# Kernel optimization log

Measured on AMD Instinct MI355X. Metric: run time of the kernel, lower is better.

The kernel has to match this reference:

```python
import jax, jax.numpy as jnp
import numpy as np


def _shift_kernels():
    # [4,1,3,3] OIHW: left, right, up, down shift-difference kernels (as in torch module)
    kl = [[0, 0, 0], [-1, 1, 0], [0, 0, 0]]
    kr = [[0, 0, 0], [0, 1, -1], [0, 0, 0]]
    ku = [[0, -1, 0], [0, 1, 0], [0, 0, 0]]
    kd = [[0, 0, 0], [0, 1, 0], [0, -1, 0]]
    return jnp.asarray(np.stack([kl, kr, ku, kd])[:, None], dtype=jnp.float32)


def _avgpool4(x):
    # x: [B,1,H,W] -> [B,1,H//4,W//4], non-overlapping 4x4 mean (nn.AvgPool2d(4))
    b, c, h, w = x.shape
    return x.reshape(b, c, h // 4, 4, w // 4, 4).mean(axis=(3, 5))


def setup_inputs() -> dict:
    key = jax.random.key(0)
    k1, k2 = jax.random.split(key)
    org = jax.random.uniform(k1, (32, 3, 512, 512), dtype=jnp.float32)
    enhance = jax.random.uniform(k2, (32, 3, 512, 512), dtype=jnp.float32)
    return {"org": org, "enhance": enhance}


def reference(org, enhance):
    org_pool = _avgpool4(jnp.mean(org, axis=1, keepdims=True))
    enh_pool = _avgpool4(jnp.mean(enhance, axis=1, keepdims=True))
    # conv is linear, so D_org_k - D_enh_k == conv(org_pool - enh_pool, k).
    diff = org_pool - enh_pool  # [B,1,h,w]
    d = jax.lax.conv_general_dilated(
        diff, _shift_kernels(), window_strides=(1, 1),
        padding=((1, 1), (1, 1)),
        dimension_numbers=("NCHW", "OIHW", "NCHW"))  # [B,4,h,w]
    # torch: mean(D_left + D_right + D_up + D_down) over [B,1,h,w]
    return jnp.mean(jnp.sum(d * d, axis=1))
```

## Files before the change

kernel.cpp:

```cpp
#include <hip/hip_runtime.h>

#define NB 32
#define NC 3
#define NH 512
#define NW 512
#define PH 128
#define PW 128
#define NPOOL (NB * PH * PW)
#define NBLK_POOL (NPOOL / 256)
#define NBLK_RED  (NPOOL / 256)

__global__ __launch_bounds__(256) void pool_diff_kernel(
    const float* __restrict__ org, const float* __restrict__ enh,
    float* __restrict__ pooled)
{
    int idx = blockIdx.x * blockDim.x + threadIdx.x;
    int pw = idx & (PW - 1);
    int ph = (idx >> 7) & (PH - 1);
    int b  = idx >> 14;

    const float4* o4 = (const float4*)org;
    const float4* e4 = (const float4*)enh;
    const int rowF4 = NW / 4;
    const int chanF4 = NH * rowF4;

    int base = (b * NC * NH + 4 * ph) * rowF4 + pw;

    float4 o[12], e[12];
#pragma unroll
    for (int c = 0; c < NC; ++c) {
#pragma unroll
        for (int dy = 0; dy < 4; ++dy) {
            int off = base + c * chanF4 + dy * rowF4;
            o[c * 4 + dy] = o4[off];
            e[c * 4 + dy] = e4[off];
        }
    }

    float4 a0, a1, a2, a3;
    a0.x = o[0].x - e[0].x; a0.y = o[0].y - e[0].y; a0.z = o[0].z - e[0].z; a0.w = o[0].w - e[0].w;
    a1.x = o[1].x - e[1].x; a1.y = o[1].y - e[1].y; a1.z = o[1].z - e[1].z; a1.w = o[1].w - e[1].w;
    a2.x = o[2].x - e[2].x; a2.y = o[2].y - e[2].y; a2.z = o[2].z - e[2].z; a2.w = o[2].w - e[2].w;
    a3.x = o[3].x - e[3].x; a3.y = o[3].y - e[3].y; a3.z = o[3].z - e[3].z; a3.w = o[3].w - e[3].w;
#pragma unroll
    for (int i = 4; i < 12; i += 4) {
        a0.x += o[i].x - e[i].x;     a0.y += o[i].y - e[i].y;     a0.z += o[i].z - e[i].z;     a0.w += o[i].w - e[i].w;
        a1.x += o[i+1].x - e[i+1].x; a1.y += o[i+1].y - e[i+1].y; a1.z += o[i+1].z - e[i+1].z; a1.w += o[i+1].w - e[i+1].w;
        a2.x += o[i+2].x - e[i+2].x; a2.y += o[i+2].y - e[i+2].y; a2.z += o[i+2].z - e[i+2].z; a2.w += o[i+2].w - e[i+2].w;
        a3.x += o[i+3].x - e[i+3].x; a3.y += o[i+3].y - e[i+3].y; a3.z += o[i+3].z - e[i+3].z; a3.w += o[i+3].w - e[i+3].w;
    }
    float acc = ((a0.x + a1.x) + (a2.x + a3.x)) + ((a0.y + a1.y) + (a2.y + a3.y))
              + ((a0.z + a1.z) + (a2.z + a3.z)) + ((a0.w + a1.w) + (a2.w + a3.w));

    pooled[idx] = acc * (1.0f / 48.0f);
}

__global__ __launch_bounds__(256) void spa_reduce_kernel(
    const float* __restrict__ pooled, float* __restrict__ partials)
{
    int idx = blockIdx.x * blockDim.x + threadIdx.x;
    int pw = idx & (PW - 1);
    int ph = (idx >> 7) & (PH - 1);
    int b  = idx >> 14;
    const float* img = pooled + b * (PH * PW);

    float c = img[ph * PW + pw];
    float l = (pw > 0)      ? img[ph * PW + pw - 1] : 0.f;
    float r = (pw < PW - 1) ? img[ph * PW + pw + 1] : 0.f;
    float u = (ph > 0)      ? img[(ph - 1) * PW + pw] : 0.f;
    float d = (ph < PH - 1) ? img[(ph + 1) * PW + pw] : 0.f;

    float dl = c - l, dr = c - r, du = c - u, dd = c - d;
    float s = (dl * dl + dr * dr) + (du * du + dd * dd);

#pragma unroll
    for (int off = 32; off > 0; off >>= 1)
        s += __shfl_down(s, off, 64);

    __shared__ float smem[4];
    int lane = threadIdx.x & 63;
    int wid  = threadIdx.x >> 6;
    if (lane == 0) smem[wid] = s;
    __syncthreads();
    if (threadIdx.x == 0)
        partials[blockIdx.x] = (smem[0] + smem[1]) + (smem[2] + smem[3]);
}

__global__ __launch_bounds__(256) void final_reduce_kernel(
    const float* __restrict__ partials, float* __restrict__ out)
{
    float s = 0.f;
#pragma unroll
    for (int i = 0; i < NBLK_RED / 256; ++i)
        s += partials[i * 256 + threadIdx.x];

#pragma unroll
    for (int off = 32; off > 0; off >>= 1)
        s += __shfl_down(s, off, 64);

    __shared__ float smem[4];
    int lane = threadIdx.x & 63;
    int wid  = threadIdx.x >> 6;
    if (lane == 0) smem[wid] = s;
    __syncthreads();
    if (threadIdx.x == 0)
        out[0] = ((smem[0] + smem[1]) + (smem[2] + smem[3])) * (1.0f / (float)NPOOL);
}

extern "C" void kernel_launch(void* const* d_in, const int* in_sizes, int n_in,
                              void* d_out, int out_size, void* d_ws, size_t ws_size,
                              hipStream_t stream) {
    const float* org = (const float*)d_in[0];
    const float* enh = (const float*)d_in[1];
    float* out = (float*)d_out;
    float* pooled   = (float*)d_ws;
    float* partials = (float*)d_ws + NPOOL;

    pool_diff_kernel<<<NBLK_POOL, 256, 0, stream>>>(org, enh, pooled);
    spa_reduce_kernel<<<NBLK_RED, 256, 0, stream>>>(pooled, partials);
    final_reduce_kernel<<<1, 256, 0, stream>>>(partials, out);
}
```

Measured before the change: 215.7 us.

## Split pooling per channel plane and sum channels in stencil kernel

The pooling kernel now gives each thread one channel's 4x4 window instead of all three channels. That triples the thread count and cuts per-thread register use from 24 float4 loads to 8. Per-channel partial pools go to a workspace three times larger, and the stencil kernel sums the three planes on the fly. In exchange, the stencil kernel makes five times three scattered reads, and the intermediate traffic grows.

```diff
diff --git a/kernel.cpp b/kernel.cpp
--- a/kernel.cpp
+++ b/kernel.cpp
@@ -6,69 +6,61 @@
 #define NW 512
 #define PH 128
 #define PW 128
-#define NPOOL (NB * PH * PW)
-#define NBLK_POOL (NPOOL / 256)
-#define NBLK_RED  (NPOOL / 256)
+#define NPOOL  (NB * PH * PW)
+#define NPLANE (NB * NC)
+#define PLANE_ELEMS (PH * PW)
+#define NBLK_A (NPLANE * NH / 8)
+#define NBLK_RED (NPOOL / 256)
 
-__global__ __launch_bounds__(256) void pool_diff_kernel(
-    const float* __restrict__ org, const float* __restrict__ enh,
-    float* __restrict__ pooled)
+__global__ __launch_bounds__(256) void stageA_pool_kernel(
+    const float4* __restrict__ o4, const float4* __restrict__ e4,
+    float* __restrict__ partial)
+{
+    int t   = threadIdx.x;
+    int x4  = t & 127;
+    int phl = t >> 7;
+    int base = blockIdx.x * 1024 + phl * 512 + x4;
+
+    float4 o0 = o4[base];
+    float4 o1 = o4[base + 128];
+    float4 o2 = o4[base + 256];
+    float4 o3 = o4[base + 384];
+    float4 e0 = e4[base];
+    float4 e1 = e4[base + 128];
+    float4 e2 = e4[base + 256];
+    float4 e3 = e4[base + 384];
+
+    float4 d;
+    d.x = ((o0.x - e0.x) + (o1.x - e1.x)) + ((o2.x - e2.x) + (o3.x - e3.x));
+    d.y = ((o0.y - e0.y) + (o1.y - e1.y)) + ((o2.y - e2.y) + (o3.y - e3.y));
+    d.z = ((o0.z - e0.z) + (o1.z - e1.z)) + ((o2.z - e2.z) + (o3.z - e3.z));
+    d.w = ((o0.w - e0.w) + (o1.w - e1.w)) + ((o2.w - e2.w) + (o3.w - e3.w));
+    float v = (d.x + d.y) + (d.z + d.w);
+
+    int plane = blockIdx.x >> 6;
+    int prow  = ((blockIdx.x & 63) << 1) | phl;
+    partial[plane * PLANE_ELEMS + prow * PW + x4] = v * (1.0f / 48.0f);
+}
+
+__global__ __launch_bounds__(256) void spa_reduce_kernel(
+    const float* __restrict__ partial, float* __restrict__ partials_out)
 {
     int idx = blockIdx.x * blockDim.x + threadIdx.x;
     int pw = idx & (PW - 1);
     int ph = (idx >> 7) & (PH - 1);
     int b  = idx >> 14;
 
-    const float4* o4 = (const float4*)org;
-    const float4* e4 = (const float4*)enh;
-    const int rowF4 = NW / 4;
-    const int chanF4 = NH * rowF4;
+    const float* p0 = partial + (b * 3 + 0) * PLANE_ELEMS;
+    const float* p1 = partial + (b * 3 + 1) * PLANE_ELEMS;
+    const float* p2 = partial + (b * 3 + 2) * PLANE_ELEMS;
 
-    int base = (b * NC * NH + 4 * ph) * rowF4 + pw;
-
-    float4 o[12], e[12];
-#pragma unroll
-    for (int c = 0; c < NC; ++c) {
-#pragma unroll
-        for (int dy = 0; dy < 4; ++dy) {
-            int off = base + c * chanF4 + dy * rowF4;
-            o[c * 4 + dy] = o4[off];
-            e[c * 4 + dy] = e4[off];
-        }
-    }
-
-    float4 a0, a1, a2, a3;
-    a0.x = o[0].x - e[0].x; a0.y = o[0].y - e[0].y; a0.z = o[0].z - e[0].z; a0.w = o[0].w - e[0].w;
-    a1.x = o[1].x - e[1].x; a1.y = o[1].y - e[1].y; a1.z = o[1].z - e[1].z; a1.w = o[1].w - e[1].w;
-    a2.x = o[2].x - e[2].x; a2.y = o[2].y - e[2].y; a2.z = o[2].z - e[2].z; a2.w = o[2].w - e[2].w;
-    a3.x = o[3].x - e[3].x; a3.y = o[3].y - e[3].y; a3.z = o[3].z - e[3].z; a3.w = o[3].w - e[3].w;
-#pragma unroll
-    for (int i = 4; i < 12; i += 4) {
-        a0.x += o[i].x - e[i].x;     a0.y += o[i].y - e[i].y;     a0.z += o[i].z - e[i].z;     a0.w += o[i].w - e[i].w;
-        a1.x += o[i+1].x - e[i+1].x; a1.y += o[i+1].y - e[i+1].y; a1.z += o[i+1].z - e[i+1].z; a1.w += o[i+1].w - e[i+1].w;
-        a2.x += o[i+2].x - e[i+2].x; a2.y += o[i+2].y - e[i+2].y; a2.z += o[i+2].z - e[i+2].z; a2.w += o[i+2].w - e[i+2].w;
-        a3.x += o[i+3].x - e[i+3].x; a3.y += o[i+3].y - e[i+3].y; a3.z += o[i+3].z - e[i+3].z; a3.w += o[i+3].w - e[i+3].w;
-    }
-    float acc = ((a0.x + a1.x) + (a2.x + a3.x)) + ((a0.y + a1.y) + (a2.y + a3.y))
-              + ((a0.z + a1.z) + (a2.z + a3.z)) + ((a0.w + a1.w) + (a2.w + a3.w));
-
-    pooled[idx] = acc * (1.0f / 48.0f);
-}
-
-__global__ __launch_bounds__(256) void spa_reduce_kernel(
-    const float* __restrict__ pooled, float* __restrict__ partials)
-{
-    int idx = blockIdx.x * blockDim.x + threadIdx.x;
-    int pw = idx & (PW - 1);
-    int ph = (idx >> 7) & (PH - 1);
-    int b  = idx >> 14;
-    const float* img = pooled + b * (PH * PW);
-
-    float c = img[ph * PW + pw];
-    float l = (pw > 0)      ? img[ph * PW + pw - 1] : 0.f;
-    float r = (pw < PW - 1) ? img[ph * PW + pw + 1] : 0.f;
-    float u = (ph > 0)      ? img[(ph - 1) * PW + pw] : 0.f;
-    float d = (ph < PH - 1) ? img[(ph + 1) * PW + pw] : 0.f;
+    #define POOLED(y, x) (p0[(y) * PW + (x)] + p1[(y) * PW + (x)] + p2[(y) * PW + (x)])
+    float c = POOLED(ph, pw);
+    float l = (pw > 0)      ? POOLED(ph, pw - 1) : 0.f;
+    float r = (pw < PW - 1) ? POOLED(ph, pw + 1) : 0.f;
+    float u = (ph > 0)      ? POOLED(ph - 1, pw) : 0.f;
+    float d = (ph < PH - 1) ? POOLED(ph + 1, pw) : 0.f;
+    #undef POOLED
 
     float dl = c - l, dr = c - r, du = c - u, dd = c - d;
     float s = (dl * dl + dr * dr) + (du * du + dd * dd);
@@ -83,7 +75,7 @@
     if (lane == 0) smem[wid] = s;
     __syncthreads();
     if (threadIdx.x == 0)
-        partials[blockIdx.x] = (smem[0] + smem[1]) + (smem[2] + smem[3]);
+        partials_out[blockIdx.x] = (smem[0] + smem[1]) + (smem[2] + smem[3]);
 }
 
 __global__ __launch_bounds__(256) void final_reduce_kernel(
@@ -110,13 +102,13 @@
 extern "C" void kernel_launch(void* const* d_in, const int* in_sizes, int n_in,
                               void* d_out, int out_size, void* d_ws, size_t ws_size,
                               hipStream_t stream) {
-    const float* org = (const float*)d_in[0];
-    const float* enh = (const float*)d_in[1];
+    const float4* o4 = (const float4*)d_in[0];
+    const float4* e4 = (const float4*)d_in[1];
     float* out = (float*)d_out;
-    float* pooled   = (float*)d_ws;
-    float* partials = (float*)d_ws + NPOOL;
+    float* partial      = (float*)d_ws;
+    float* blockpartial = (float*)d_ws + NPLANE * PLANE_ELEMS;
 
-    pool_diff_kernel<<<NBLK_POOL, 256, 0, stream>>>(org, enh, pooled);
-    spa_reduce_kernel<<<NBLK_RED, 256, 0, stream>>>(pooled, partials);
-    final_reduce_kernel<<<1, 256, 0, stream>>>(partials, out);
+    stageA_pool_kernel<<<NBLK_A, 256, 0, stream>>>(o4, e4, partial);
+    spa_reduce_kernel<<<NBLK_RED, 256, 0, stream>>>(partial, blockpartial);
+    final_reduce_kernel<<<1, 256, 0, stream>>>(blockpartial, out);
 }
```

Result: no change. 213.7 us (-0.9%).
